# Optimization experiments

Hardware: AMD Instinct MI355X
Metric: run time of the kernel (lower is better)

The kernel has to match this reference:

```python
import jax, jax.numpy as jnp
import numpy as np

N = 100000
H = 8      # heads
C = 8      # out channels per head
NEG_SLOPE = 0.2
EPS = 1e-16


def setup_inputs() -> dict:
    key = jax.random.key(0)
    k1, k2, k3, k4, k5, k6 = jax.random.split(key, 6)
    x = jax.random.normal(k1, (N, 128), dtype=jnp.float32)
    edge_index = jax.random.randint(k2, (2, 1600000), 0, N, dtype=jnp.int64)
    W = jax.random.normal(k3, (128, H * C), dtype=jnp.float32) * (1.0 / np.sqrt(128))
    att_src = jax.random.normal(k4, (H, C), dtype=jnp.float32)
    att_dst = jax.random.normal(k5, (H, C), dtype=jnp.float32)
    bias = jax.random.normal(k6, (H * C,), dtype=jnp.float32) * 0.01
    return {"x": x, "edge_index": edge_index, "W": W,
            "att_src": att_src, "att_dst": att_dst, "bias": bias}


def _gat_forward(x, edge_index, W, att_src, att_dst, bias):
    # add self loops (PyG GATConv default add_self_loops=True)
    loop = jnp.arange(N, dtype=edge_index.dtype)
    src = jnp.concatenate([edge_index[0], loop])
    dst = jnp.concatenate([edge_index[1], loop])

    h = (x @ W).reshape(N, H, C)                       # [N,H,C]
    a_src = jnp.sum(h * att_src, axis=-1)              # [N,H]
    a_dst = jnp.sum(h * att_dst, axis=-1)              # [N,H]

    e = a_src[src] + a_dst[dst]                        # [E,H]
    e = jnp.where(e > 0, e, NEG_SLOPE * e)             # leaky_relu(0.2)

    # segment softmax over edges grouped by destination node
    m = jax.ops.segment_max(e, dst, num_segments=N)    # [N,H]
    m = jnp.where(jnp.isfinite(m), m, 0.0)
    ex = jnp.exp(e - m[dst])                           # [E,H]
    denom = jax.ops.segment_sum(ex, dst, num_segments=N)
    alpha = ex / (denom[dst] + EPS)                    # [E,H]

    msg = alpha[:, :, None] * h[src]                   # [E,H,C]
    out = jax.ops.segment_sum(msg, dst, num_segments=N)  # [N,H,C]
    out = out.reshape(N, H * C) + bias
    return jax.nn.relu(out)


def reference(x, edge_index, W, att_src, att_dst, bias):
    return _gat_forward(x, edge_index, W, att_src, att_dst, bias)
```

## Files before the change

kernel.cpp:

```cpp
#include <hip/hip_runtime.h>
#include <hip/hip_bf16.h>

#define NNODES 100000
#define NH 8
#define OUTD 64
#define FDIM 128
#define NEG_SLOPE 0.2f
#define NBUCK ((NNODES + 255) / 256)
#define MAXB 5376
#define CH 8192
#define ROWS_PB 128
#define NFB ((NNODES + ROWS_PB - 1) / ROWS_PB)
#define SHST 68

typedef __attribute__((ext_vector_type(8))) short bf16x8;
typedef __attribute__((ext_vector_type(4))) float f32x4;
typedef __attribute__((ext_vector_type(4))) unsigned int u32x4;

static __device__ __forceinline__ unsigned short f2bf(float f) {
    __hip_bfloat16 b = __float2bfloat16(f);
    return *(unsigned short*)&b;
}

__global__ void k_wprep(const float* __restrict__ W, unsigned short* __restrict__ wimg)
{
    int i = blockIdx.x * 256 + threadIdx.x;
    if (i >= FDIM * OUTD) return;
    int k = i >> 6, col = i & 63;
    int chs = (k >> 3) ^ (col & 15);
    wimg[col * FDIM + chs * 8 + (k & 7)] = f2bf(W[i]);
}

__global__ __launch_bounds__(256) void k_feat(
    const float* __restrict__ x, const unsigned short* __restrict__ wimg,
    const float* __restrict__ att_s, const float* __restrict__ att_d,
    __hip_bfloat16* __restrict__ h, float* __restrict__ asrc,
    float* __restrict__ adst)
{
    __shared__ unsigned short sx[ROWS_PB * FDIM];
    __shared__ unsigned short swt[OUTD * FDIM];
    __shared__ float shf[4 * 16 * SHST];
    __shared__ float sAs[OUTD], sAd[OUTD];

    int tid = threadIdx.x;
    if (tid < OUTD) { sAs[tid] = att_s[tid]; sAd[tid] = att_d[tid]; }

    {
        const u32x4* src = (const u32x4*)wimg;
        u32x4* dst = (u32x4*)swt;
        for (int i = tid; i < (OUTD * FDIM) / 8; i += 256) dst[i] = src[i];
    }
    int row0 = blockIdx.x * ROWS_PB;
    for (int c = tid; c < ROWS_PB * 16; c += 256) {
        int row = c >> 4, chunk = c & 15;
        int grow = row0 + row;
        unsigned short tmp[8];
        if (grow < NNODES) {
            const float* p = x + (size_t)grow * FDIM + chunk * 8;
            f32x4 f0 = *(const f32x4*)p;
            f32x4 f1 = *(const f32x4*)(p + 4);
#pragma unroll
            for (int j = 0; j < 4; ++j) tmp[j] = f2bf(f0[j]);
#pragma unroll
            for (int j = 0; j < 4; ++j) tmp[4 + j] = f2bf(f1[j]);
        } else {
#pragma unroll
            for (int j = 0; j < 8; ++j) tmp[j] = 0;
        }
        int chs = chunk ^ (row & 15);
        *(bf16x8*)&sx[row * FDIM + chs * 8] = *(bf16x8*)tmp;
    }
    __syncthreads();

    int w = tid >> 6, l = tid & 63;
    int l4 = l & 15, g = l >> 4;

    bf16x8 bfrag[16];
#pragma unroll
    for (int n = 0; n < 4; ++n)
#pragma unroll
        for (int kk = 0; kk < 4; ++kk) {
            int col = n * 16 + l4;
            int chs = (kk * 4 + g) ^ l4;
            bfrag[n * 4 + kk] = *(const bf16x8*)&swt[col * FDIM + chs * 8];
        }

    float* mysh = &shf[w * 16 * SHST];

#pragma unroll
    for (int rt = 0; rt < 2; ++rt) {
        int lbase = w * 32 + rt * 16;
        f32x4 acc[4];
#pragma unroll
        for (int n = 0; n < 4; ++n) acc[n] = (f32x4){0.f, 0.f, 0.f, 0.f};

#pragma unroll
        for (int kk = 0; kk < 4; ++kk) {
            int row = lbase + l4;
            int chs = (kk * 4 + g) ^ l4;
            bf16x8 a = *(const bf16x8*)&sx[row * FDIM + chs * 8];
#pragma unroll
            for (int n = 0; n < 4; ++n)
                acc[n] = __builtin_amdgcn_mfma_f32_16x16x32_bf16(
                    a, bfrag[n * 4 + kk], acc[n], 0, 0, 0);
        }

#pragma unroll
        for (int n = 0; n < 4; ++n)
#pragma unroll
            for (int r = 0; r < 4; ++r)
                mysh[(g * 4 + r) * SHST + n * 16 + l4] = acc[n][r];

#pragma unroll
        for (int i = 0; i < 2; ++i) {
            int c = i * 64 + l;
            int row = c >> 3, ch = c & 7;
            int grow = row0 + lbase + row;
            if (grow < NNODES) {
                const float* rp = &mysh[row * SHST + ch * 8];
                unsigned short tmp[8];
#pragma unroll
                for (int j = 0; j < 8; ++j) tmp[j] = f2bf(rp[j]);
                *(bf16x8*)&h[(size_t)grow * OUTD + ch * 8] = *(bf16x8*)tmp;
            }
        }
#pragma unroll
        for (int i = 0; i < 2; ++i) {
            int t = i * 64 + l;
            int row = t >> 3, hd = t & 7;
            int grow = row0 + lbase + row;
            if (grow < NNODES) {
                const float* rp = &mysh[row * SHST + hd * 8];
                float s1 = 0.f, s2 = 0.f;
#pragma unroll
                for (int j = 0; j < 8; ++j) {
                    s1 = fmaf(rp[j], sAs[hd * 8 + j], s1);
                    s2 = fmaf(rp[j], sAd[hd * 8 + j], s2);
                }
                asrc[grow * NH + hd] = s1;
                adst[grow * NH + hd] = s2;
            }
        }
    }
}

__global__ __launch_bounds__(256) void k_bin(
    const int* __restrict__ ei, int E, int* __restrict__ gCur,
    unsigned int* __restrict__ gSorted)
{
    __shared__ int cnt[NBUCK];
    __shared__ int base[NBUCK];
    int tot = E + NNODES;
    int e0 = blockIdx.x * CH;
    int e1 = e0 + CH; if (e1 > tot) e1 = tot;

    for (int i = threadIdx.x; i < NBUCK; i += 256) cnt[i] = 0;
    __syncthreads();

    for (int i = e0 + threadIdx.x; i < e1; i += 256) {
        int d = (i < E) ? ei[E + i] : (i - E);
        atomicAdd(&cnt[d >> 8], 1);
    }
    __syncthreads();

    for (int i = threadIdx.x; i < NBUCK; i += 256) {
        int c = cnt[i];
        base[i] = (c > 0) ? atomicAdd(&gCur[i], c) : 0;
        cnt[i] = 0;
    }
    __syncthreads();

    for (int i = e0 + threadIdx.x; i < e1; i += 256) {
        int s, d;
        if (i < E) { s = ei[i]; d = ei[E + i]; }
        else       { s = d = i - E; }
        int b = d >> 8;
        int p = base[b] + atomicAdd(&cnt[b], 1);
        if (p < MAXB)
            gSorted[(size_t)b * MAXB + p] =
                ((unsigned int)(d & 255) << 17) | (unsigned int)s;
    }
}

__global__ __launch_bounds__(256) void k_csr(
    const int* __restrict__ gCur, unsigned int* __restrict__ gSorted,
    int2* __restrict__ rows)
{
    __shared__ unsigned int ent[MAXB];
    __shared__ int cnt[256], cur[256];
    __shared__ int wsum[4];
    int b = blockIdx.x;
    int n = gCur[b]; if (n > MAXB) n = MAXB;
    size_t gbase = (size_t)b * MAXB;
    int tid = threadIdx.x;

    for (int i = tid; i < n; i += 256) ent[i] = gSorted[gbase + i];
    cnt[tid] = 0;
    __syncthreads();

    for (int i = tid; i < n; i += 256)
        atomicAdd(&cnt[ent[i] >> 17], 1);
    __syncthreads();

    int v = cnt[tid];
    int lane = tid & 63, wid = tid >> 6;
    int acc = v;
#pragma unroll
    for (int off = 1; off < 64; off <<= 1) {
        int t = __shfl_up(acc, off);
        if (lane >= off) acc += t;
    }
    if (lane == 63) wsum[wid] = acc;
    __syncthreads();
    int woff = 0;
#pragma unroll
    for (int i = 0; i < 4; ++i) woff += (i < wid) ? wsum[i] : 0;
    int ex = acc + woff - v;

    int node = (b << 8) + tid;
    if (node < NNODES)
        rows[node] = make_int2((int)gbase + ex, (int)gbase + ex + v);
    cur[tid] = ex;
    __syncthreads();

    for (int i = tid; i < n; i += 256) {
        unsigned int p = ent[i];
        int pos = atomicAdd(&cur[p >> 17], 1);
        gSorted[gbase + pos] = p & 0x1FFFFu;
    }
}

__global__ __launch_bounds__(256) void k_gather(
    const int2* __restrict__ rows, const unsigned int* __restrict__ esrc,
    const __hip_bfloat16* __restrict__ h, const float* __restrict__ asrc,
    const float* __restrict__ adst, const float* __restrict__ bias,
    float* __restrict__ out)
{
    int node = (blockIdx.x * 256 + threadIdx.x) >> 6;
    if (node >= NNODES) return;
    int lane = threadIdx.x & 63;
    int l5 = lane >> 5;
    int c  = lane & 31;
    int hh = c >> 2;

    float adh = adst[(unsigned)(node * NH + hh)];
    int2 se = rows[node];
    int start = se.x, end = se.y;
    const unsigned* hu = (const unsigned*)h;

    float num0 = 0.f, num1 = 0.f, den = 0.f;

    for (int base = start; base < end; base += 64) {
        int cnt = end - base; if (cnt > 64) cnt = 64;
        int sj = (base + lane < end) ? (int)esrc[base + lane] : 0;

        auto pair = [&](int k) {
            int s2 = __shfl(sj, k + l5);
            float a = asrc[(unsigned)(s2 * NH + hh)];
            unsigned w = hu[(unsigned)(s2 * 32 + c)];
            float e = a + adh;
            e = fmaxf(e, NEG_SLOPE * e);
            float ex = __expf(e);
            den += ex;
            union { unsigned u; float f; } lo, hi;
            lo.u = w << 16; hi.u = w & 0xffff0000u;
            num0 = fmaf(ex, lo.f, num0);
            num1 = fmaf(ex, hi.f, num1);
        };

        int k = 0;
        for (; k + 8 <= cnt; k += 8) {
            int sA = __shfl(sj, k + 0 + l5);
            int sB = __shfl(sj, k + 2 + l5);
            int sC = __shfl(sj, k + 4 + l5);
            int sD = __shfl(sj, k + 6 + l5);
            float aA = asrc[(unsigned)(sA * NH + hh)];
            float aB = asrc[(unsigned)(sB * NH + hh)];
            float aC = asrc[(unsigned)(sC * NH + hh)];
            float aD = asrc[(unsigned)(sD * NH + hh)];
            unsigned wA = hu[(unsigned)(sA * 32 + c)];
            unsigned wB = hu[(unsigned)(sB * 32 + c)];
            unsigned wC = hu[(unsigned)(sC * 32 + c)];
            unsigned wD = hu[(unsigned)(sD * 32 + c)];
            float eA = aA + adh; eA = fmaxf(eA, NEG_SLOPE * eA); eA = __expf(eA);
            float eB = aB + adh; eB = fmaxf(eB, NEG_SLOPE * eB); eB = __expf(eB);
            float eC = aC + adh; eC = fmaxf(eC, NEG_SLOPE * eC); eC = __expf(eC);
            float eD = aD + adh; eD = fmaxf(eD, NEG_SLOPE * eD); eD = __expf(eD);
            den += eA; den += eB; den += eC; den += eD;
            union { unsigned u; float f; } lo, hi;
            lo.u = wA << 16; hi.u = wA & 0xffff0000u;
            num0 = fmaf(eA, lo.f, num0); num1 = fmaf(eA, hi.f, num1);
            lo.u = wB << 16; hi.u = wB & 0xffff0000u;
            num0 = fmaf(eB, lo.f, num0); num1 = fmaf(eB, hi.f, num1);
            lo.u = wC << 16; hi.u = wC & 0xffff0000u;
            num0 = fmaf(eC, lo.f, num0); num1 = fmaf(eC, hi.f, num1);
            lo.u = wD << 16; hi.u = wD & 0xffff0000u;
            num0 = fmaf(eD, lo.f, num0); num1 = fmaf(eD, hi.f, num1);
        }
        for (; k + 2 <= cnt; k += 2) { pair(k); }
        if (k < cnt) {
            int s2 = __shfl(sj, k);
            float a = asrc[(unsigned)(s2 * NH + hh)];
            unsigned w = hu[(unsigned)(s2 * 32 + c)];
            float e = a + adh;
            e = fmaxf(e, NEG_SLOPE * e);
            float ex = l5 ? 0.f : __expf(e);
            den += ex;
            union { unsigned u; float f; } lo, hi;
            lo.u = w << 16; hi.u = w & 0xffff0000u;
            num0 = fmaf(ex, lo.f, num0);
            num1 = fmaf(ex, hi.f, num1);
        }
    }

    num0 += __shfl_xor(num0, 32);
    num1 += __shfl_xor(num1, 32);
    den  += __shfl_xor(den, 32);

    int ch = c * 2 + l5;
    float inv = 1.f / (den + 1e-16f);
    float vv = (l5 ? num1 : num0) * inv + bias[ch];
    out[(unsigned)(node * OUTD + ch)] = vv > 0.f ? vv : 0.f;
}

extern "C" void kernel_launch(void* const* d_in, const int* in_sizes, int n_in,
                              void* d_out, int out_size, void* d_ws, size_t ws_size,
                              hipStream_t stream)
{
    const float* x     = (const float*)d_in[0];
    const int*   ei    = (const int*)  d_in[1];
    const float* W     = (const float*)d_in[2];
    const float* att_s = (const float*)d_in[3];
    const float* att_d = (const float*)d_in[4];
    const float* bias  = (const float*)d_in[5];
    float* out = (float*)d_out;
    int E = in_sizes[1] / 2;
    int tot = E + NNODES;

    __hip_bfloat16* h = (__hip_bfloat16*)d_ws;
    float* asrc   = (float*)(h + (size_t)NNODES * OUTD);
    float* adst   = asrc + (size_t)NNODES * NH;
    int2*  rows   = (int2*)(adst + (size_t)NNODES * NH);
    int*   gCur   = (int*)(rows + NNODES);
    unsigned int* gSorted = (unsigned int*)(gCur + 512);
    unsigned short* wimg  = (unsigned short*)(gSorted + (size_t)NBUCK * MAXB);

    hipMemsetAsync(gCur, 0, 512 * sizeof(int), stream);

    k_wprep<<<(FDIM * OUTD + 255) / 256, 256, 0, stream>>>(W, wimg);
    k_feat<<<NFB, 256, 0, stream>>>(x, wimg, att_s, att_d, h, asrc, adst);
    k_bin<<<(tot + CH - 1) / CH, 256, 0, stream>>>(ei, E, gCur, gSorted);
    k_csr<<<NBUCK, 256, 0, stream>>>(gCur, gSorted, rows);
    k_gather<<<(NNODES * 64 + 255) / 256, 256, 0, stream>>>(
        rows, gSorted, h, asrc, adst, bias, out);
}
```

Measured before the change: 124.9 us.

## Fuse weight prep into feature kernel and widen gather to four edges per wave

```diff
diff --git a/kernel.cpp b/kernel.cpp
--- a/kernel.cpp
+++ b/kernel.cpp
@@ -15,24 +15,14 @@
 
 typedef __attribute__((ext_vector_type(8))) short bf16x8;
 typedef __attribute__((ext_vector_type(4))) float f32x4;
-typedef __attribute__((ext_vector_type(4))) unsigned int u32x4;
 
 static __device__ __forceinline__ unsigned short f2bf(float f) {
     __hip_bfloat16 b = __float2bfloat16(f);
     return *(unsigned short*)&b;
 }
 
-__global__ void k_wprep(const float* __restrict__ W, unsigned short* __restrict__ wimg)
-{
-    int i = blockIdx.x * 256 + threadIdx.x;
-    if (i >= FDIM * OUTD) return;
-    int k = i >> 6, col = i & 63;
-    int chs = (k >> 3) ^ (col & 15);
-    wimg[col * FDIM + chs * 8 + (k & 7)] = f2bf(W[i]);
-}
-
 __global__ __launch_bounds__(256) void k_feat(
-    const float* __restrict__ x, const unsigned short* __restrict__ wimg,
+    const float* __restrict__ x, const float* __restrict__ W,
     const float* __restrict__ att_s, const float* __restrict__ att_d,
     __hip_bfloat16* __restrict__ h, float* __restrict__ asrc,
     float* __restrict__ adst)
@@ -45,10 +35,14 @@
     int tid = threadIdx.x;
     if (tid < OUTD) { sAs[tid] = att_s[tid]; sAd[tid] = att_d[tid]; }
 
-    {
-        const u32x4* src = (const u32x4*)wimg;
-        u32x4* dst = (u32x4*)swt;
-        for (int i = tid; i < (OUTD * FDIM) / 8; i += 256) dst[i] = src[i];
+    for (int i = tid; i < OUTD * 16; i += 256) {
+        int col = i & 63, chunk = i >> 6;
+        unsigned short tmp[8];
+#pragma unroll
+        for (int j = 0; j < 8; ++j)
+            tmp[j] = f2bf(W[(chunk * 8 + j) * OUTD + col]);
+        int chs = chunk ^ (col & 15);
+        *(bf16x8*)&swt[col * FDIM + chs * 8] = *(bf16x8*)tmp;
     }
     int row0 = blockIdx.x * ROWS_PB;
     for (int c = tid; c < ROWS_PB * 16; c += 256) {
@@ -239,88 +233,73 @@
     int node = (blockIdx.x * 256 + threadIdx.x) >> 6;
     if (node >= NNODES) return;
     int lane = threadIdx.x & 63;
-    int l5 = lane >> 5;
-    int c  = lane & 31;
-    int hh = c >> 2;
+    int slot = lane >> 4;
+    int li   = lane & 15;
+    int hh   = li >> 1;
 
     float adh = adst[(unsigned)(node * NH + hh)];
     int2 se = rows[node];
-    int start = se.x, end = se.y;
-    const unsigned* hu = (const unsigned*)h;
-
-    float num0 = 0.f, num1 = 0.f, den = 0.f;
-
-    for (int base = start; base < end; base += 64) {
-        int cnt = end - base; if (cnt > 64) cnt = 64;
-        int sj = (base + lane < end) ? (int)esrc[base + lane] : 0;
-
-        auto pair = [&](int k) {
-            int s2 = __shfl(sj, k + l5);
-            float a = asrc[(unsigned)(s2 * NH + hh)];
-            unsigned w = hu[(unsigned)(s2 * 32 + c)];
-            float e = a + adh;
-            e = fmaxf(e, NEG_SLOPE * e);
-            float ex = __expf(e);
-            den += ex;
-            union { unsigned u; float f; } lo, hi;
-            lo.u = w << 16; hi.u = w & 0xffff0000u;
-            num0 = fmaf(ex, lo.f, num0);
-            num1 = fmaf(ex, hi.f, num1);
-        };
+    const uint2* hu = (const uint2*)h;
+
+    float n0 = 0.f, n1 = 0.f, n2 = 0.f, n3 = 0.f, den = 0.f;
+
+    for (int base = se.x; base < se.y; base += 64) {
+        int cnt = se.y - base; if (cnt > 64) cnt = 64;
+        int sj = (lane < cnt) ? (int)esrc[base + lane] : 0;
 
         int k = 0;
         for (; k + 8 <= cnt; k += 8) {
-            int sA = __shfl(sj, k + 0 + l5);
-            int sB = __shfl(sj, k + 2 + l5);
-            int sC = __shfl(sj, k + 4 + l5);
-            int sD = __shfl(sj, k + 6 + l5);
+            int sA = __shfl(sj, k + slot);
+            int sB = __shfl(sj, k + 4 + slot);
             float aA = asrc[(unsigned)(sA * NH + hh)];
             float aB = asrc[(unsigned)(sB * NH + hh)];
-            float aC = asrc[(unsigned)(sC * NH + hh)];
-            float aD = asrc[(unsigned)(sD * NH + hh)];
-            unsigned wA = hu[(unsigned)(sA * 32 + c)];
-            unsigned wB = hu[(unsigned)(sB * 32 + c)];
-            unsigned wC = hu[(unsigned)(sC * 32 + c)];
-            unsigned wD = hu[(unsigned)(sD * 32 + c)];
+            uint2 wA = hu[(unsigned)(sA * 16 + li)];
+            uint2 wB = hu[(unsigned)(sB * 16 + li)];
             float eA = aA + adh; eA = fmaxf(eA, NEG_SLOPE * eA); eA = __expf(eA);
             float eB = aB + adh; eB = fmaxf(eB, NEG_SLOPE * eB); eB = __expf(eB);
-            float eC = aC + adh; eC = fmaxf(eC, NEG_SLOPE * eC); eC = __expf(eC);
-            float eD = aD + adh; eD = fmaxf(eD, NEG_SLOPE * eD); eD = __expf(eD);
-            den += eA; den += eB; den += eC; den += eD;
-            union { unsigned u; float f; } lo, hi;
-            lo.u = wA << 16; hi.u = wA & 0xffff0000u;
-            num0 = fmaf(eA, lo.f, num0); num1 = fmaf(eA, hi.f, num1);
-            lo.u = wB << 16; hi.u = wB & 0xffff0000u;
-            num0 = fmaf(eB, lo.f, num0); num1 = fmaf(eB, hi.f, num1);
-            lo.u = wC << 16; hi.u = wC & 0xffff0000u;
-            num0 = fmaf(eC, lo.f, num0); num1 = fmaf(eC, hi.f, num1);
-            lo.u = wD << 16; hi.u = wD & 0xffff0000u;
-            num0 = fmaf(eD, lo.f, num0); num1 = fmaf(eD, hi.f, num1);
-        }
-        for (; k + 2 <= cnt; k += 2) { pair(k); }
-        if (k < cnt) {
-            int s2 = __shfl(sj, k);
+            den += eA; den += eB;
+            union { unsigned u; float f; } t;
+            t.u = wA.x << 16;         n0 = fmaf(eA, t.f, n0);
+            t.u = wA.x & 0xffff0000u; n1 = fmaf(eA, t.f, n1);
+            t.u = wA.y << 16;         n2 = fmaf(eA, t.f, n2);
+            t.u = wA.y & 0xffff0000u; n3 = fmaf(eA, t.f, n3);
+            t.u = wB.x << 16;         n0 = fmaf(eB, t.f, n0);
+            t.u = wB.x & 0xffff0000u; n1 = fmaf(eB, t.f, n1);
+            t.u = wB.y << 16;         n2 = fmaf(eB, t.f, n2);
+            t.u = wB.y & 0xffff0000u; n3 = fmaf(eB, t.f, n3);
+        }
+        for (; k < cnt; k += 4) {
+            int s2 = __shfl(sj, k + slot);
+            bool valid = (k + slot) < cnt;
             float a = asrc[(unsigned)(s2 * NH + hh)];
-            unsigned w = hu[(unsigned)(s2 * 32 + c)];
-            float e = a + adh;
-            e = fmaxf(e, NEG_SLOPE * e);
-            float ex = l5 ? 0.f : __expf(e);
+            uint2 w = hu[(unsigned)(s2 * 16 + li)];
+            float e = a + adh; e = fmaxf(e, NEG_SLOPE * e);
+            float ex = valid ? __expf(e) : 0.f;
             den += ex;
-            union { unsigned u; float f; } lo, hi;
-            lo.u = w << 16; hi.u = w & 0xffff0000u;
-            num0 = fmaf(ex, lo.f, num0);
-            num1 = fmaf(ex, hi.f, num1);
-        }
-    }
-
-    num0 += __shfl_xor(num0, 32);
-    num1 += __shfl_xor(num1, 32);
-    den  += __shfl_xor(den, 32);
-
-    int ch = c * 2 + l5;
-    float inv = 1.f / (den + 1e-16f);
-    float vv = (l5 ? num1 : num0) * inv + bias[ch];
-    out[(unsigned)(node * OUTD + ch)] = vv > 0.f ? vv : 0.f;
+            union { unsigned u; float f; } t;
+            t.u = w.x << 16;         n0 = fmaf(ex, t.f, n0);
+            t.u = w.x & 0xffff0000u; n1 = fmaf(ex, t.f, n1);
+            t.u = w.y << 16;         n2 = fmaf(ex, t.f, n2);
+            t.u = w.y & 0xffff0000u; n3 = fmaf(ex, t.f, n3);
+        }
+    }
+
+    n0 += __shfl_xor(n0, 16); n0 += __shfl_xor(n0, 32);
+    n1 += __shfl_xor(n1, 16); n1 += __shfl_xor(n1, 32);
+    n2 += __shfl_xor(n2, 16); n2 += __shfl_xor(n2, 32);
+    n3 += __shfl_xor(n3, 16); n3 += __shfl_xor(n3, 32);
+    den += __shfl_xor(den, 16); den += __shfl_xor(den, 32);
+
+    if (slot == 0) {
+        float inv = 1.f / (den + 1e-16f);
+        int ch = li * 4;
+        float4 v;
+        v.x = fmaxf(n0 * inv + bias[ch + 0], 0.f);
+        v.y = fmaxf(n1 * inv + bias[ch + 1], 0.f);
+        v.z = fmaxf(n2 * inv + bias[ch + 2], 0.f);
+        v.w = fmaxf(n3 * inv + bias[ch + 3], 0.f);
+        *(float4*)&out[(unsigned)(node * OUTD + ch)] = v;
+    }
 }
 
 extern "C" void kernel_launch(void* const* d_in, const int* in_sizes, int n_in,
@@ -343,12 +322,10 @@
     int2*  rows   = (int2*)(adst + (size_t)NNODES * NH);
     int*   gCur   = (int*)(rows + NNODES);
     unsigned int* gSorted = (unsigned int*)(gCur + 512);
-    unsigned short* wimg  = (unsigned short*)(gSorted + (size_t)NBUCK * MAXB);
 
     hipMemsetAsync(gCur, 0, 512 * sizeof(int), stream);
 
-    k_wprep<<<(FDIM * OUTD + 255) / 256, 256, 0, stream>>>(W, wimg);
-    k_feat<<<NFB, 256, 0, stream>>>(x, wimg, att_s, att_d, h, asrc, adst);
+    k_feat<<<NFB, 256, 0, stream>>>(x, W, att_s, att_d, h, asrc, adst);
     k_bin<<<(tot + CH - 1) / CH, 256, 0, stream>>>(ei, E, gCur, gSorted);
     k_csr<<<NBUCK, 256, 0, stream>>>(gCur, gSorted, rows);
     k_gather<<<(NNODES * 64 + 255) / 256, 256, 0, stream>>>(
```

Result: faster. 122.0 us (-2.3%).
